# Kernel tuning notes

Hardware: AMD Instinct MI355X
Metric: run time of the kernel (lower is better)

The kernel has to match this reference:

```python
import jax, jax.numpy as jnp
import numpy as np

N_NODES = 100000
N_EDGES = 3200000
# (out_dim, in_dim) for the 4 BayesianLinear layers: mlp1 = [5->16, 16->32], mlp2 = [35->16, 16->1]
LAYER_DIMS = [(16, 5), (32, 16), (16, 35), (1, 16)]


def setup_inputs() -> dict:
    key = jax.random.key(0)
    ks = iter(jax.random.split(key, 32))
    inp = {}
    inp["x"] = jax.random.normal(next(ks), (N_NODES, 3), jnp.float32)
    inp["edge_attr"] = jax.random.normal(next(ks), (N_EDGES, 2), jnp.float32)
    inp["edge_index"] = jax.random.randint(next(ks), (2, N_EDGES), 0, N_NODES, dtype=jnp.int64)
    for li, (o, i) in enumerate(LAYER_DIMS, 1):
        inp[f"l{li}_wmu"] = jax.random.normal(next(ks), (o, i), jnp.float32) * 0.1
        inp[f"l{li}_wrho"] = jax.random.normal(next(ks), (o, i), jnp.float32) * 0.1 - 5.0
        inp[f"l{li}_bmu"] = jax.random.normal(next(ks), (o,), jnp.float32) * 0.1
        inp[f"l{li}_brho"] = jax.random.normal(next(ks), (o,), jnp.float32) * 0.1 - 5.0
        inp[f"l{li}_eps_w"] = jax.random.normal(next(ks), (o, i), jnp.float32)
        inp[f"l{li}_eps_b"] = jax.random.normal(next(ks), (o,), jnp.float32)
    return inp


def _bayes_linear(h, wmu, wrho, bmu, brho, eps_w, eps_b):
    # sampled weight: W = mu + softplus(rho) * eps  (blitz BayesianLinear)
    W = wmu + jax.nn.softplus(wrho) * eps_w          # [out, in]
    b = bmu + jax.nn.softplus(brho) * eps_b          # [out]
    return h @ W.T + b


def _igconv(x, edge_index, edge_attr, p1, p2, p3, p4):
    src, dst = edge_index[0], edge_index[1]          # x_j = x[src], aggregate at dst
    x_j = x[src]                                     # [E, 3] irregular gather
    m = jnp.concatenate([x_j, edge_attr], axis=1)    # [E, 5]
    m = jax.nn.relu(_bayes_linear(m, *p1))           # [E, 16]
    m = jax.nn.relu(_bayes_linear(m, *p2))           # [E, 32]
    agg = jax.ops.segment_max(m, dst, num_segments=x.shape[0])  # [N, 32]
    agg = jnp.where(jnp.isneginf(agg), 0.0, agg)     # nodes with no in-edges -> 0
    h = jnp.concatenate([x, agg], axis=1)            # [N, 35]
    h = jax.nn.relu(_bayes_linear(h, *p3))           # [N, 16]
    comb = jax.nn.sigmoid(_bayes_linear(h, *p4))     # [N, 1]
    return jnp.concatenate([x[:, :2], comb], axis=1) # [N, 3]


def reference(x, edge_attr, edge_index,
              l1_wmu, l1_wrho, l1_bmu, l1_brho, l1_eps_w, l1_eps_b,
              l2_wmu, l2_wrho, l2_bmu, l2_brho, l2_eps_w, l2_eps_b,
              l3_wmu, l3_wrho, l3_bmu, l3_brho, l3_eps_w, l3_eps_b,
              l4_wmu, l4_wrho, l4_bmu, l4_brho, l4_eps_w, l4_eps_b):
    p1 = (l1_wmu, l1_wrho, l1_bmu, l1_brho, l1_eps_w, l1_eps_b)
    p2 = (l2_wmu, l2_wrho, l2_bmu, l2_brho, l2_eps_w, l2_eps_b)
    p3 = (l3_wmu, l3_wrho, l3_bmu, l3_brho, l3_eps_w, l3_eps_b)
    p4 = (l4_wmu, l4_wrho, l4_bmu, l4_brho, l4_eps_w, l4_eps_b)
    h = x
    for _ in range(3):  # three stacked applications of the same IGConv
        h = _igconv(h, edge_index, edge_attr, p1, p2, p3, p4)
    return h
```

## Files before the change

### kernel.cpp

```cpp
#include <hip/hip_runtime.h>
#include <math.h>

#define WTOT  1233
#define PKOFS 1280
#define PKTOT 352

typedef __fp16 h2 __attribute__((ext_vector_type(2)));
typedef __fp16 f16x8 __attribute__((ext_vector_type(8)));
typedef float f32x16 __attribute__((ext_vector_type(16)));

__device__ __forceinline__ h2 u2h(unsigned int u) { return __builtin_bit_cast(h2, u); }
__device__ __forceinline__ unsigned int h2u(h2 h) { return __builtin_bit_cast(unsigned int, h); }
#define DOT2(a, b, c) __builtin_amdgcn_fdot2((a), (b), (c), false)

__device__ __forceinline__ float softplus_f(float x) {
  return fmaxf(x, 0.f) + log1pf(expf(-fabsf(x)));
}

struct PrepArgs {
  const float* wmu[4]; const float* wrho[4]; const float* epsw[4];
  const float* bmu[4]; const float* brho[4]; const float* epsb[4];
  float* out; int* bucketCur; int* etot; int nbuck;
};

__global__ void prep_all_kernel(PrepArgs a) {
  const int wsz[4] = {80, 512, 560, 16};
  const int wof[4] = {0, 96, 640, 1216};
  const int bsz[4] = {16, 32, 16, 1};
  const int bof[4] = {80, 608, 1200, 1232};
  float* wg = a.out;
  int tid = threadIdx.x;
  if (tid < a.nbuck) a.bucketCur[tid] = 0;
  if (tid == 1023) *a.etot = 0;
#pragma unroll
  for (int l = 0; l < 4; l++) {
    for (int i = tid; i < wsz[l]; i += 1024)
      wg[wof[l] + i] = a.wmu[l][i] + softplus_f(a.wrho[l][i]) * a.epsw[l][i];
    for (int i = tid; i < bsz[l]; i += 1024)
      wg[bof[l] + i] = a.bmu[l][i] + softplus_f(a.brho[l][i]) * a.epsb[l][i];
  }
  __syncthreads();
  unsigned int* wp = (unsigned int*)(wg + PKOFS);
  int t = tid;
  if (t < 16) {
    wp[t]      = h2u(h2{(__fp16)wg[t * 5 + 0], (__fp16)wg[t * 5 + 1]});
    wp[16 + t] = h2u(h2{(__fp16)wg[t * 5 + 2], (__fp16)0.f});
    wp[32 + t] = h2u(h2{(__fp16)wg[t * 5 + 3], (__fp16)wg[t * 5 + 4]});
    ((float*)wp)[304 + t] = wg[80 + t];
  }
  if (t < 32) {
    ((float*)wp)[320 + t] = wg[608 + t];
    for (int j = 0; j < 8; j++)
      wp[48 + t * 8 + j] =
          h2u(h2{(__fp16)wg[96 + t * 16 + 2 * j], (__fp16)wg[96 + t * 16 + 2 * j + 1]});
  }
}

__global__ __launch_bounds__(1024) void bhist_kernel(const int* __restrict__ dst,
                                                     int* __restrict__ bucketCur,
                                                     int E, int NBUCK) {
  __shared__ int h[1024];
  int tid = threadIdx.x;
  for (int i = tid; i < NBUCK; i += 1024) h[i] = 0;
  __syncthreads();
  int base = blockIdx.x * 8192;
#pragma unroll
  for (int r = 0; r < 2; r++) {
    int e = base + r * 4096 + tid * 4;
    if (e + 3 < E) {
      int4 d4v = *(const int4*)(dst + e);
      atomicAdd(&h[d4v.x >> 8], 1);
      atomicAdd(&h[d4v.y >> 8], 1);
      atomicAdd(&h[d4v.z >> 8], 1);
      atomicAdd(&h[d4v.w >> 8], 1);
    } else {
      for (int k = 0; k < 4; k++)
        if (e + k < E) atomicAdd(&h[dst[e + k] >> 8], 1);
    }
  }
  __syncthreads();
  for (int i = tid; i < NBUCK; i += 1024) {
    int c = h[i];
    if (c) atomicAdd(&bucketCur[i], c);
  }
}

__global__ __launch_bounds__(1024) void scanBk_kernel(int* __restrict__ bucketCur,
                                                      int* __restrict__ bucketOff,
                                                      int NBUCK) {
  __shared__ int wsum[16];
  __shared__ int woff[16];
  int tid = threadIdx.x, lane = tid & 63, wid = tid >> 6;
  int v = (tid < NBUCK) ? bucketCur[tid] : 0;
  int x = v;
#pragma unroll
  for (int off = 1; off < 64; off <<= 1) {
    int t = __shfl_up(x, off, 64);
    if (lane >= off) x += t;
  }
  if (lane == 63) wsum[wid] = x;
  __syncthreads();
  if (wid == 0) {
    int s = (lane < 16) ? wsum[lane] : 0;
#pragma unroll
    for (int off = 1; off < 16; off <<= 1) {
      int t = __shfl_up(s, off, 64);
      if (lane >= off) s += t;
    }
    if (lane < 16) woff[lane] = s - wsum[lane];
  }
  __syncthreads();
  int excl = woff[wid] + x - v;
  if (tid < NBUCK) {
    bucketOff[tid] = excl;
    bucketCur[tid] = excl;
    if (tid == NBUCK - 1) bucketOff[NBUCK] = excl + v;
  }
}

__global__ __launch_bounds__(1024) void part_kernel(
    const int* __restrict__ src, const int* __restrict__ dst,
    const float2* __restrict__ ea, int* __restrict__ bucketCur,
    uint2* __restrict__ brec8, int E, int NBUCK) {
  __shared__ int h[1024];
  int tid = threadIdx.x;
  for (int i = tid; i < NBUCK; i += 1024) h[i] = 0;
  __syncthreads();
  int base = blockIdx.x * 8192;
  int d[8], s[8];
  unsigned int a[8];
  bool v[8];
#pragma unroll
  for (int j = 0; j < 8; j++) {
    int e = base + j * 1024 + tid;
    v[j] = e < E;
    if (v[j]) {
      d[j] = dst[e];
      s[j] = src[e];
      float2 t = ea[e];
      a[j] = h2u(__builtin_amdgcn_cvt_pkrtz(t.x, t.y));
      atomicAdd(&h[d[j] >> 8], 1);
    }
  }
  __syncthreads();
  for (int i = tid; i < NBUCK; i += 1024) {
    int c = h[i];
    h[i] = c ? atomicAdd(&bucketCur[i], c) : 0;
  }
  __syncthreads();
#pragma unroll
  for (int j = 0; j < 8; j++) {
    if (v[j]) {
      int pos = atomicAdd(&h[d[j] >> 8], 1);
      brec8[pos] = make_uint2(a[j], (unsigned int)s[j] | ((unsigned int)(d[j] & 255) << 24));
    }
  }
}

__global__ __launch_bounds__(1024) void scat_kernel(
    const uint2* __restrict__ brec8, const int* __restrict__ bucketOff,
    int* __restrict__ etot, uint2* __restrict__ se8, unsigned int* __restrict__ d4,
    int N) {
  __shared__ int cnt[256];
  __shared__ int sstart[256];
  __shared__ int wsum[4];
  __shared__ int woff[4];
  __shared__ int sbase;
  int b = blockIdx.x, tid = threadIdx.x;
  int lane = tid & 63, wid = tid >> 6;
  if (tid < 256) cnt[tid] = 0;
  __syncthreads();
  int e0 = bucketOff[b], e1 = bucketOff[b + 1];
  for (int i = e0 + tid; i < e1; i += 1024) atomicAdd(&cnt[brec8[i].y >> 24], 1);
  __syncthreads();
  int v = 0;
  if (tid < 256) v = (cnt[tid] + 3) & ~3;
  int x = v;
#pragma unroll
  for (int off = 1; off < 64; off <<= 1) {
    int t = __shfl_up(x, off, 64);
    if (lane >= off) x += t;
  }
  if (tid < 256 && lane == 63) wsum[wid] = x;
  __syncthreads();
  if (wid == 0 && lane < 4) {
    int s = wsum[lane];
#pragma unroll
    for (int off = 1; off < 4; off <<= 1) {
      int t = __shfl_up(s, off, 64);
      if (lane >= off) s += t;
    }
    woff[lane] = s - wsum[lane];
    if (lane == 3) sbase = atomicAdd(etot, s);
  }
  __syncthreads();
  if (tid < 256) {
    int start = sbase + woff[wid] + x - v;
    sstart[tid] = start;
    cnt[tid] = start;
  }
  __syncthreads();
  for (int i = e0 + tid; i < e1; i += 1024) {
    uint2 t = brec8[i];
    int pos = atomicAdd(&cnt[t.y >> 24], 1);
    se8[pos] = make_uint2(t.y & 0x00FFFFFFu, t.x);
  }
  __syncthreads();
  if (tid < 256) {
    int node = b * 256 + tid;
    int start = sstart[tid];
    int endR = cnt[tid];
    int endP = start + ((endR - start + 3) & ~3);
    if (endR > start) {
      uint2 rep = se8[start];
      for (int k = endR; k < endP; k++) se8[k] = rep;
      for (int k = start; k < endP; k += 4) d4[k >> 2] = (unsigned int)node;
    }
  }
}

__global__ void xpack_kernel(const float* __restrict__ x, uint2* __restrict__ xpk,
                             unsigned int* __restrict__ agg32, int n) {
  int i = blockIdx.x * blockDim.x + threadIdx.x;
  if (i < n) {
    h2 a = __builtin_amdgcn_cvt_pkrtz(x[3 * i], x[3 * i + 1]);
    h2 b = __builtin_amdgcn_cvt_pkrtz(x[3 * i + 2], 0.f);
    xpk[i] = make_uint2(h2u(a), h2u(b));
    uint4 z = make_uint4(0u, 0u, 0u, 0u);
    uint4* ap = (uint4*)(agg32 + (size_t)i * 32);
#pragma unroll
    for (int k = 0; k < 8; k++) ap[k] = z;
    if (i == 0) {
      uint4* as = (uint4*)(agg32 + (size_t)n * 32);
#pragma unroll
      for (int k = 0; k < 8; k++) as[k] = z;
    }
  }
}

__global__ __launch_bounds__(256) void edge_kernel(
    const uint2* __restrict__ xpk, const uint2* __restrict__ se8,
    const unsigned int* __restrict__ d4, unsigned int* __restrict__ agg32,
    const float* __restrict__ wg, const int* __restrict__ pEtot,
    unsigned int tag, int N) {
  __shared__ __align__(16) unsigned int lds[4][64][12];
  const unsigned int* wp = (const unsigned int*)(wg + PKOFS);
  const float* bf = (const float*)wp;
  const int Etot = *pEtot;
  if (blockIdx.x * 256 >= Etot) return;
  const int tid = threadIdx.x;
  const int lane = tid & 63;
  const int wslot = tid >> 6;
  const int e = blockIdx.x * 256 + tid;

  bool vld = e < Etot;
  uint2 se = vld ? se8[e] : make_uint2(0u, 0u);
  int d = vld ? (int)d4[e >> 2] : N;
  uint2 xs = xpk[se.x];

  h2 p01 = u2h(xs.x), p2v = u2h(xs.y), pea = u2h(se.y);
  unsigned int m1[8];
#pragma unroll
  for (int p = 0; p < 8; p++) {
    const int oA = 2 * p, oB = 2 * p + 1;
    float sA = DOT2(p01, u2h(wp[oA]),
                DOT2(p2v, u2h(wp[16 + oA]),
                DOT2(pea, u2h(wp[32 + oA]), bf[304 + oA])));
    float sB = DOT2(p01, u2h(wp[oB]),
                DOT2(p2v, u2h(wp[16 + oB]),
                DOT2(pea, u2h(wp[32 + oB]), bf[304 + oB])));
    m1[p] = h2u(__builtin_amdgcn_cvt_pkrtz(fmaxf(sA, 0.f), fmaxf(sB, 0.f)));
  }

  uint4* rowp = (uint4*)&lds[wslot][lane][0];
  rowp[0] = make_uint4(m1[0], m1[1], m1[2], m1[3]);
  rowp[1] = make_uint4(m1[4], m1[5], m1[6], m1[7]);
  asm volatile("s_waitcnt lgkmcnt(0)" ::: "memory");
  __builtin_amdgcn_sched_barrier(0);

  const int col = lane & 31;
  const int h = lane >> 5;
  f16x8 bfrag = __builtin_bit_cast(f16x8, *(const uint4*)&wp[48 + col * 8 + 4 * h]);
  float bias = bf[320 + col];
  f32x16 cini;
#pragma unroll
  for (int i = 0; i < 16; i++) cini[i] = bias;

  __builtin_amdgcn_s_setprio(1);
  f16x8 a0 = __builtin_bit_cast(f16x8, *(const uint4*)&lds[wslot][col][4 * h]);
  f16x8 a1 = __builtin_bit_cast(f16x8, *(const uint4*)&lds[wslot][32 + col][4 * h]);
  f32x16 acc0 = __builtin_amdgcn_mfma_f32_32x32x16_f16(a0, bfrag, cini, 0, 0, 0);
  f32x16 acc1 = __builtin_amdgcn_mfma_f32_32x32x16_f16(a1, bfrag, cini, 0, 0, 0);

  float bm[2][4];
#pragma unroll
  for (int q = 0; q < 4; q++) {
    bm[0][q] = fmaxf(fmaxf(acc0[4 * q], acc0[4 * q + 1]),
                     fmaxf(acc0[4 * q + 2], fmaxf(acc0[4 * q + 3], 0.f)));
    bm[1][q] = fmaxf(fmaxf(acc1[4 * q], acc1[4 * q + 1]),
                     fmaxf(acc1[4 * q + 2], fmaxf(acc1[4 * q + 3], 0.f)));
  }
  __builtin_amdgcn_s_setprio(0);

  int dp4 = __shfl_up(d, 4, 64);
  bool isHead = ((lane & 3) == 0) && (lane == 0 || d != dp4);
  unsigned long long hm = __ballot(isHead);

  unsigned long long rem = hm;
  while (rem) {
    int a = (int)__builtin_ctzll(rem);
    rem &= rem - 1;
    int b = rem ? (int)__builtin_ctzll(rem) : 64;
    int rd = __shfl(d, a, 64);
    int A = a >> 2, B = b >> 2;
    float mx = 0.f;
#pragma unroll
    for (int g = 0; g < 2; g++) {
#pragma unroll
      for (int q = 0; q < 4; q++) {
        int blk = 8 * g + 2 * q + h;
        bool in = (blk >= A) && (blk < B);
        mx = fmaxf(mx, in ? bm[g][q] : 0.f);
      }
    }
    mx = fmaxf(mx, __shfl_xor(mx, 32, 64));
    if (lane < 32 && rd < N) {
      unsigned int bits = __float_as_uint(mx);
      atomicMax(agg32 + (size_t)rd * 32 + col, (tag << 30) | (bits >> 1));
    }
  }
}

__global__ __launch_bounds__(256) void node_kernel(
    const float* __restrict__ x, const float* __restrict__ cin,
    float* __restrict__ cout, uint2* __restrict__ xpk,
    float* __restrict__ outFinal, const unsigned int* __restrict__ agg32,
    const float* __restrict__ wg, unsigned int tag, int n) {
  int nid = blockIdx.x * blockDim.x + threadIdx.x;
  if (nid >= n) return;
  const uint4* ap = (const uint4*)(agg32 + (size_t)nid * 32);
  uint4 q[8];
#pragma unroll
  for (int i = 0; i < 8; i++) q[i] = ap[i];
  float av[32];
#pragma unroll
  for (int i = 0; i < 8; i++) {
    unsigned int w[4] = {q[i].x, q[i].y, q[i].z, q[i].w};
#pragma unroll
    for (int j = 0; j < 4; j++) {
      unsigned int u = ((w[j] >> 30) == tag) ? ((w[j] & 0x3FFFFFFFu) << 1) : 0u;
      av[4 * i + j] = __uint_as_float(u);
    }
  }
  float x0 = x[3 * nid], x1 = x[3 * nid + 1];
  float x2 = cin ? cin[nid] : x[3 * nid + 2];
  float h[16];
#pragma unroll
  for (int o = 0; o < 16; o++) {
    float sa = wg[1200 + o];
    sa = fmaf(wg[640 + o * 35 + 0], x0, sa);
    sa = fmaf(wg[640 + o * 35 + 1], x1, sa);
    sa = fmaf(wg[640 + o * 35 + 2], x2, sa);
#pragma unroll
    for (int k = 0; k < 32; k++) sa = fmaf(wg[640 + o * 35 + 3 + k], av[k], sa);
    h[o] = fmaxf(sa, 0.f);
  }
  float z4 = wg[1232];
#pragma unroll
  for (int k = 0; k < 16; k++) z4 = fmaf(wg[1216 + k], h[k], z4);
  float comb = 1.f / (1.f + expf(-z4));
  cout[nid] = comb;
  ((unsigned int*)xpk)[2 * nid + 1] = h2u(__builtin_amdgcn_cvt_pkrtz(comb, 0.f));
  if (outFinal) {
    outFinal[3 * nid] = x0;
    outFinal[3 * nid + 1] = x1;
    outFinal[3 * nid + 2] = comb;
  }
}

extern "C" void kernel_launch(void* const* d_in, const int* in_sizes, int n_in,
                              void* d_out, int out_size, void* d_ws, size_t ws_size,
                              hipStream_t stream) {
  const float* x = (const float*)d_in[0];
  const float* ea = (const float*)d_in[1];
  const int* eidx = (const int*)d_in[2];
  const int N = in_sizes[0] / 3;
  const int E = in_sizes[1] / 2;
  const int* src = eidx;
  const int* dst = eidx + E;
  const int NBUCK = (N + 255) >> 8;
  const int EP = E + 3 * N;

  char* p = (char*)d_ws;
  size_t off = 0;
  auto alloc = [&](size_t bytes) -> char* {
    char* r = p + off;
    off = (off + bytes + 255) & ~(size_t)255;
    return r;
  };
  float* wbuf = (float*)alloc((size_t)(PKOFS + PKTOT) * 4);
  int* bucketOff = (int*)alloc(((size_t)NBUCK + 1) * 4);
  int* bucketCur = (int*)alloc((size_t)NBUCK * 4);
  int* etot = (int*)alloc(4);
  uint2* se8 = (uint2*)alloc((size_t)EP * 8);
  unsigned int* d4 = (unsigned int*)alloc(((size_t)(EP + 3) / 4 + 1) * 4);
  char* uni = alloc((size_t)E * 8);
  uint2* brec8 = (uint2*)uni;
  size_t uoff = 0;
  auto ualloc = [&](size_t bytes) -> char* {
    char* r = uni + uoff;
    uoff = (uoff + bytes + 255) & ~(size_t)255;
    return r;
  };
  unsigned int* agg32 = (unsigned int*)ualloc(((size_t)N + 1) * 32 * 4);
  uint2* xpk = (uint2*)ualloc((size_t)N * 8);
  float* bufA = (float*)ualloc((size_t)N * 4);
  float* bufB = (float*)ualloc((size_t)N * 4);
  (void)ws_size;

  PrepArgs pa;
  for (int l = 0; l < 4; l++) {
    pa.wmu[l] = (const float*)d_in[3 + 6 * l + 0];
    pa.wrho[l] = (const float*)d_in[3 + 6 * l + 1];
    pa.bmu[l] = (const float*)d_in[3 + 6 * l + 2];
    pa.brho[l] = (const float*)d_in[3 + 6 * l + 3];
    pa.epsw[l] = (const float*)d_in[3 + 6 * l + 4];
    pa.epsb[l] = (const float*)d_in[3 + 6 * l + 5];
  }
  pa.out = wbuf;
  pa.bucketCur = bucketCur;
  pa.etot = etot;
  pa.nbuck = NBUCK;

  const int TB = 256;
  auto blocks = [&](int n) { return dim3((n + TB - 1) / TB); };

  prep_all_kernel<<<dim3(1), dim3(1024), 0, stream>>>(pa);
  bhist_kernel<<<dim3((E + 8191) / 8192), dim3(1024), 0, stream>>>(dst, bucketCur, E, NBUCK);
  scanBk_kernel<<<dim3(1), dim3(1024), 0, stream>>>(bucketCur, bucketOff, NBUCK);
  part_kernel<<<dim3((E + 8191) / 8192), dim3(1024), 0, stream>>>(
      src, dst, (const float2*)ea, bucketCur, brec8, E, NBUCK);
  scat_kernel<<<dim3(NBUCK), dim3(1024), 0, stream>>>(brec8, bucketOff, etot, se8, d4, N);
  xpack_kernel<<<blocks(N), dim3(TB), 0, stream>>>(x, xpk, agg32, N);

  float* outp = (float*)d_out;
  const int ebp = (EP + 255) / 256;
  edge_kernel<<<dim3(ebp), dim3(TB), 0, stream>>>(xpk, se8, d4, agg32, wbuf, etot, 1u, N);
  node_kernel<<<blocks(N), dim3(TB), 0, stream>>>(x, nullptr, bufA, xpk, nullptr,
                                                  agg32, wbuf, 1u, N);
  edge_kernel<<<dim3(ebp), dim3(TB), 0, stream>>>(xpk, se8, d4, agg32, wbuf, etot, 2u, N);
  node_kernel<<<blocks(N), dim3(TB), 0, stream>>>(x, bufA, bufB, xpk, nullptr,
                                                  agg32, wbuf, 2u, N);
  edge_kernel<<<dim3(ebp), dim3(TB), 0, stream>>>(xpk, se8, d4, agg32, wbuf, etot, 3u, N);
  node_kernel<<<blocks(N), dim3(TB), 0, stream>>>(x, bufB, bufA, xpk, outp,
                                                  agg32, wbuf, 3u, N);
}
```

Measured before the change: 339.9 us.

## Stage scatter output in LDS and fold xpack into histogram kernel

The scatter kernel now builds each bucket's sorted edge records and per-quad destination ids in shared memory, then writes them to global memory with coalesced 16-byte stores. This replaces the scattered 8-byte global writes and padding fix-ups, and falls back to the old path when a bucket exceeds the staging capacity. The x packing and agg32 zeroing move into the histogram kernel, which removes one launch, and agg32/xpk get their own workspace instead of aliasing the partition buffer. The large LDS allocation (about 110 KB) limits occupancy of the scatter kernel.

```diff
diff --git a/kernel.cpp b/kernel.cpp
--- a/kernel.cpp
+++ b/kernel.cpp
@@ -4,6 +4,8 @@
 #define WTOT  1233
 #define PKOFS 1280
 #define PKTOT 352
+
+#define SCAT_CAP 12288
 
 typedef __fp16 h2 __attribute__((ext_vector_type(2)));
 typedef __fp16 f16x8 __attribute__((ext_vector_type(8)));
@@ -56,12 +58,31 @@
   }
 }
 
-__global__ __launch_bounds__(1024) void bhist_kernel(const int* __restrict__ dst,
-                                                     int* __restrict__ bucketCur,
-                                                     int E, int NBUCK) {
+__global__ __launch_bounds__(1024) void bhist_kernel(
+    const int* __restrict__ dst, int* __restrict__ bucketCur,
+    const float* __restrict__ x, uint2* __restrict__ xpk,
+    unsigned int* __restrict__ agg32, int E, int N, int NBUCK) {
   __shared__ int h[1024];
   int tid = threadIdx.x;
   for (int i = tid; i < NBUCK; i += 1024) h[i] = 0;
+  int nbase = blockIdx.x * 256;
+  if (tid < 256) {
+    int i = nbase + tid;
+    if (i < N) {
+      h2 a = __builtin_amdgcn_cvt_pkrtz(x[3 * i], x[3 * i + 1]);
+      h2 b = __builtin_amdgcn_cvt_pkrtz(x[3 * i + 2], 0.f);
+      xpk[i] = make_uint2(h2u(a), h2u(b));
+    }
+  }
+  {
+    uint4 z = make_uint4(0u, 0u, 0u, 0u);
+    uint4* ap = (uint4*)agg32;
+    size_t lim = ((size_t)N + 1) * 8;
+    size_t i0 = (size_t)nbase * 8 + tid;
+    if (i0 < lim) ap[i0] = z;
+    size_t i1 = i0 + 1024;
+    if (i1 < (size_t)(nbase + 256) * 8 && i1 < lim) ap[i1] = z;
+  }
   __syncthreads();
   int base = blockIdx.x * 8192;
 #pragma unroll
@@ -166,6 +187,9 @@
   __shared__ int wsum[4];
   __shared__ int woff[4];
   __shared__ int sbase;
+  __shared__ int ptot;
+  __shared__ __align__(16) uint2 stage[SCAT_CAP];
+  __shared__ unsigned int staged4[SCAT_CAP / 4];
   int b = blockIdx.x, tid = threadIdx.x;
   int lane = tid & 63, wid = tid >> 6;
   if (tid < 256) cnt[tid] = 0;
@@ -191,49 +215,66 @@
       if (lane >= off) s += t;
     }
     woff[lane] = s - wsum[lane];
-    if (lane == 3) sbase = atomicAdd(etot, s);
-  }
-  __syncthreads();
-  if (tid < 256) {
-    int start = sbase + woff[wid] + x - v;
-    sstart[tid] = start;
-    cnt[tid] = start;
-  }
-  __syncthreads();
-  for (int i = e0 + tid; i < e1; i += 1024) {
-    uint2 t = brec8[i];
-    int pos = atomicAdd(&cnt[t.y >> 24], 1);
-    se8[pos] = make_uint2(t.y & 0x00FFFFFFu, t.x);
-  }
-  __syncthreads();
-  if (tid < 256) {
-    int node = b * 256 + tid;
-    int start = sstart[tid];
-    int endR = cnt[tid];
-    int endP = start + ((endR - start + 3) & ~3);
-    if (endR > start) {
-      uint2 rep = se8[start];
-      for (int k = endR; k < endP; k++) se8[k] = rep;
-      for (int k = start; k < endP; k += 4) d4[k >> 2] = (unsigned int)node;
-    }
-  }
-}
-
-__global__ void xpack_kernel(const float* __restrict__ x, uint2* __restrict__ xpk,
-                             unsigned int* __restrict__ agg32, int n) {
-  int i = blockIdx.x * blockDim.x + threadIdx.x;
-  if (i < n) {
-    h2 a = __builtin_amdgcn_cvt_pkrtz(x[3 * i], x[3 * i + 1]);
-    h2 b = __builtin_amdgcn_cvt_pkrtz(x[3 * i + 2], 0.f);
-    xpk[i] = make_uint2(h2u(a), h2u(b));
-    uint4 z = make_uint4(0u, 0u, 0u, 0u);
-    uint4* ap = (uint4*)(agg32 + (size_t)i * 32);
-#pragma unroll
-    for (int k = 0; k < 8; k++) ap[k] = z;
-    if (i == 0) {
-      uint4* as = (uint4*)(agg32 + (size_t)n * 32);
-#pragma unroll
-      for (int k = 0; k < 8; k++) as[k] = z;
+    if (lane == 3) { ptot = s; sbase = atomicAdd(etot, s); }
+  }
+  __syncthreads();
+  int total = ptot;
+  if (total <= SCAT_CAP) {
+    if (tid < 256) {
+      int start = woff[wid] + x - v;
+      sstart[tid] = start;
+      cnt[tid] = start;
+    }
+    __syncthreads();
+    for (int i = e0 + tid; i < e1; i += 1024) {
+      uint2 t = brec8[i];
+      int pos = atomicAdd(&cnt[t.y >> 24], 1);
+      stage[pos] = make_uint2(t.y & 0x00FFFFFFu, t.x);
+    }
+    __syncthreads();
+    if (tid < 256) {
+      int start = sstart[tid];
+      int endR = cnt[tid];
+      int endP = start + ((endR - start + 3) & ~3);
+      if (endR > start) {
+        uint2 rep = stage[start];
+        for (int k = endR; k < endP; k++) stage[k] = rep;
+        unsigned int node = (unsigned int)(b * 256 + tid);
+        for (int k = start; k < endP; k += 4) staged4[k >> 2] = node;
+      }
+    }
+    __syncthreads();
+    int base = sbase;
+    uint4* dstp = (uint4*)(se8 + base);
+    const uint4* srcp = (const uint4*)stage;
+    int n4 = total >> 1;
+    for (int i = tid; i < n4; i += 1024) dstp[i] = srcp[i];
+    unsigned int* d4p = d4 + (base >> 2);
+    int nd = total >> 2;
+    for (int i = tid; i < nd; i += 1024) d4p[i] = staged4[i];
+  } else {
+    if (tid < 256) {
+      int start = sbase + woff[wid] + x - v;
+      sstart[tid] = start;
+      cnt[tid] = start;
+    }
+    __syncthreads();
+    for (int i = e0 + tid; i < e1; i += 1024) {
+      uint2 t = brec8[i];
+      int pos = atomicAdd(&cnt[t.y >> 24], 1);
+      se8[pos] = make_uint2(t.y & 0x00FFFFFFu, t.x);
+    }
+    __syncthreads();
+    if (tid < 256) {
+      int node = b * 256 + tid;
+      int start = sstart[tid];
+      int endR = cnt[tid];
+      int endP = start + ((endR - start + 3) & ~3);
+      if (endR > start) {
+        uint2 rep = se8[start];
+        for (int k = endR; k < endP; k++) se8[k] = rep;
+        for (int k = start; k < endP; k += 4) d4[k >> 2] = (unsigned int)node;
+      }
     }
   }
 }
@@ -404,18 +445,12 @@
   int* etot = (int*)alloc(4);
   uint2* se8 = (uint2*)alloc((size_t)EP * 8);
   unsigned int* d4 = (unsigned int*)alloc(((size_t)(EP + 3) / 4 + 1) * 4);
+  unsigned int* agg32 = (unsigned int*)alloc(((size_t)N + 1) * 32 * 4);
+  uint2* xpk = (uint2*)alloc((size_t)N * 8);
   char* uni = alloc((size_t)E * 8);
   uint2* brec8 = (uint2*)uni;
-  size_t uoff = 0;
-  auto ualloc = [&](size_t bytes) -> char* {
-    char* r = uni + uoff;
-    uoff = (uoff + bytes + 255) & ~(size_t)255;
-    return r;
-  };
-  unsigned int* agg32 = (unsigned int*)ualloc(((size_t)N + 1) * 32 * 4);
-  uint2* xpk = (uint2*)ualloc((size_t)N * 8);
-  float* bufA = (float*)ualloc((size_t)N * 4);
-  float* bufB = (float*)ualloc((size_t)N * 4);
+  float* bufA = (float*)uni;
+  float* bufB = (float*)(uni + (((size_t)N * 4 + 255) & ~(size_t)255));
   (void)ws_size;
 
   PrepArgs pa;
@@ -436,12 +471,17 @@
   auto blocks = [&](int n) { return dim3((n + TB - 1) / TB); };
 
   prep_all_kernel<<<dim3(1), dim3(1024), 0, stream>>>(pa);
-  bhist_kernel<<<dim3((E + 8191) / 8192), dim3(1024), 0, stream>>>(dst, bucketCur, E, NBUCK);
+  {
+    int gb = (E + 8191) / 8192;
+    int gn = (N + 255) / 256;
+    int g = gb > gn ? gb : gn;
+    bhist_kernel<<<dim3(g), dim3(1024), 0, stream>>>(dst, bucketCur, x, xpk, agg32,
+                                                     E, N, NBUCK);
+  }
   scanBk_kernel<<<dim3(1), dim3(1024), 0, stream>>>(bucketCur, bucketOff, NBUCK);
   part_kernel<<<dim3((E + 8191) / 8192), dim3(1024), 0, stream>>>(
       src, dst, (const float2*)ea, bucketCur, brec8, E, NBUCK);
   scat_kernel<<<dim3(NBUCK), dim3(1024), 0, stream>>>(brec8, bucketOff, etot, se8, d4, N);
-  xpack_kernel<<<blocks(N), dim3(TB), 0, stream>>>(x, xpk, agg32, N);
 
   float* outp = (float*)d_out;
   const int ebp = (EP + 255) / 256;
```

After: 326.4 us. 4.0% less time.
